# Kernel tuning notes

Hardware: AMD Instinct MI355X
Metric: run time of the kernel (lower is better)

Reference implementation:

```python
import jax, jax.numpy as jnp
import numpy as np

N = 50000   # total residue nodes across the batch of peptides
E = 800000  # total directed intra-peptide edges (avg degree 16)
D = 512


def _w(k, shape):
    fan_in = shape[0]
    return (jax.random.normal(k, shape, jnp.float32) / np.sqrt(fan_in)).astype(jnp.float32)


def setup_inputs() -> dict:
    key = jax.random.key(0)
    ks = jax.random.split(key, 12)
    return {
        "peptide_feature": jax.random.normal(ks[0], (N, D), jnp.float32),
        "edge_index": jax.random.randint(ks[1], (2, E), 0, N),
        # aanet_proj: 512 -> 1024 -> 1024 -> 512 -> 80 (ReLU between, none after last)
        "W1": _w(ks[2], (512, 1024)), "b1": jnp.zeros((1024,), jnp.float32),
        "W2": _w(ks[3], (1024, 1024)), "b2": jnp.zeros((1024,), jnp.float32),
        "W3": _w(ks[4], (1024, 512)), "b3": jnp.zeros((512,), jnp.float32),
        "W4": _w(ks[5], (512, 80)), "b4": jnp.zeros((80,), jnp.float32),
        # in_net: 80 -> 512
        "Win": _w(ks[6], (80, 512)), "bin_": jnp.zeros((512,), jnp.float32),
        # GIN conv MLP: 512 -> 512 -> 512 (eps = 0)
        "Wg1": _w(ks[7], (512, 512)), "bg1": jnp.zeros((512,), jnp.float32),
        "Wg2": _w(ks[8], (512, 512)), "bg2": jnp.zeros((512,), jnp.float32),
        # out_net: 512 -> 80
        "Wout": _w(ks[9], (512, 80)), "bout": jnp.zeros((80,), jnp.float32),
    }


def reference(peptide_feature, edge_index, W1, b1, W2, b2, W3, b3, W4, b4,
              Win, bin_, Wg1, bg1, Wg2, bg2, Wout, bout):
    relu = jax.nn.relu
    # aanet_proj
    h = relu(peptide_feature @ W1 + b1)
    h = relu(h @ W2 + b2)
    h = relu(h @ W3 + b3)
    peptide_feat = h @ W4 + b4                      # [N, 80]
    # in_net
    x = peptide_feat @ Win + bin_                   # [N, 512]
    # GIN message passing (sum aggregation, eps=0): per-sample loop in the
    # original is equivalent to one global pass since edges are sample-local.
    src, dst = edge_index[0], edge_index[1]
    agg = jax.ops.segment_sum(x[src], dst, num_segments=N)   # [N, 512]
    g = x + agg
    g = relu(g @ Wg1 + bg1) @ Wg2 + bg2             # GIN MLP
    # out_net
    peptide_mask = g @ Wout + bout                  # [N, 80]
    return peptide_mask, peptide_feat
```

## Files before the change

### kernel.cpp

```cpp
#include <hip/hip_runtime.h>
#include <stdint.h>


using bf16x8 = __attribute__((ext_vector_type(8))) short;
using f32x4  = __attribute__((ext_vector_type(4))) float;

__device__ inline unsigned short f2bf(float f) {
    union { float f; unsigned u; } v; v.f = f;
    unsigned u = v.u;
    u += 0x7FFFu + ((u >> 16) & 1u);
    return (unsigned short)(u >> 16);
}
__device__ inline float bf2f(unsigned u16) {
    return __uint_as_float(u16 << 16);
}

struct PreDescs {
    const float* W[8]; unsigned short* Wt[8];
    int K[8], M[8], Kp[8], ntx[8], start[8];
    int tEnd, cEnd, eEnd;
    const float* feat; unsigned short* featb; int nFeat;
    const int* ei; int E; int* cnt;
};

__global__ __launch_bounds__(256) void rg_preprocess(PreDescs d) {
    int b = blockIdx.x;
    int tid = threadIdx.x;
    if (b < d.tEnd) {
        __shared__ float t[32][33];
        int di = 0;
#pragma unroll
        for (int i = 1; i < 8; ++i) if (b >= d.start[i]) di = i;
        int local = b - d.start[di];
        int bx = local % d.ntx[di];
        int by = local / d.ntx[di];
        const float* W = d.W[di];
        unsigned short* Wt = d.Wt[di];
        int K = d.K[di], M = d.M[di], Kp = d.Kp[di];
        int mb = bx * 32, kb = by * 32;
        int tx = tid & 31, tg = tid >> 5;
#pragma unroll
        for (int p = 0; p < 4; ++p) {
            int r = tg + p * 8;
            int k = kb + r, m = mb + tx;
            t[r][tx] = (k < K && m < M) ? W[(size_t)k * M + m] : 0.f;
        }
        __syncthreads();
#pragma unroll
        for (int p = 0; p < 4; ++p) {
            int r = tg + p * 8;
            int mo = mb + r, ko = kb + tx;
            Wt[(size_t)mo * Kp + ko] = f2bf(t[tx][r]);
        }
    } else if (b < d.cEnd) {
        int i = ((b - d.tEnd) * 256 + tid) * 4;
        if (i + 3 < d.nFeat) {
            float4 v = *(const float4*)(d.feat + i);
            ushort4 o; o.x = f2bf(v.x); o.y = f2bf(v.y); o.z = f2bf(v.z); o.w = f2bf(v.w);
            *(ushort4*)(d.featb + i) = o;
        }
    } else {
        int e = (b - d.cEnd) * 256 + tid;
        if (e < d.E) atomicAdd(&d.cnt[d.ei[d.E + e]], 1);
    }
}

template <bool RELU, bool OUT_BF, bool OUT_F32, bool DEGB, int MT>
__global__ __launch_bounds__(256) void rg_gemm(
    const unsigned short* __restrict__ A, const unsigned short* __restrict__ Bt,
    const float* __restrict__ bias, const int* __restrict__ deg, int Mvalid,
    unsigned short* __restrict__ outB, float* __restrict__ outF,
    int Nrows, int Kp, int Mp, int gN)
{
    __shared__ __align__(16) unsigned short As[128 * 64];
    __shared__ __align__(16) unsigned short Bs[128 * 64];

    int bid = blockIdx.x;
    int xcd = bid & 7;
    int slot = bid >> 3;
    int c = slot % MT;
    int rsub = slot / MT;
    int rt = rsub * 8 + xcd;
    if (rt >= gN) return;
    const int rowBase = rt * 128;
    const int nBase   = c * 128;

    const int tid  = threadIdx.x;
    const int lane = tid & 63;
    const int w    = tid >> 6;
    const int wm   = w & 1, wn = w >> 1;

    f32x4 acc[4][4];
#pragma unroll
    for (int i = 0; i < 4; ++i)
#pragma unroll
        for (int j = 0; j < 4; ++j) acc[i][j] = (f32x4){0.f, 0.f, 0.f, 0.f};

    const int nkt = Kp >> 6;
    for (int kt = 0; kt < nkt; ++kt) {
        __syncthreads();
        const int k0 = kt * 64;
#pragma unroll
        for (int i = 0; i < 4; ++i) {
            int q   = i * 256 + tid;
            int r   = q >> 3;
            int cbg = (q & 7) ^ (r & 7);
            const unsigned short* gp = A + (size_t)(rowBase + r) * Kp + k0 + cbg * 8;
            __builtin_amdgcn_global_load_lds(
                (const __attribute__((address_space(1))) void*)gp,
                (__attribute__((address_space(3))) void*)(&As[q * 8]), 16, 0, 0);
        }
#pragma unroll
        for (int i = 0; i < 4; ++i) {
            int q   = i * 256 + tid;
            int r   = q >> 3;
            int cbg = (q & 7) ^ (r & 7);
            const unsigned short* gp = Bt + (size_t)(nBase + r) * Kp + k0 + cbg * 8;
            __builtin_amdgcn_global_load_lds(
                (const __attribute__((address_space(1))) void*)gp,
                (__attribute__((address_space(3))) void*)(&Bs[q * 8]), 16, 0, 0);
        }
        __syncthreads();
#pragma unroll
        for (int kk = 0; kk < 2; ++kk) {
            bf16x8 a[4], b[4];
            const int cb = kk * 4 + (lane >> 4);
#pragma unroll
            for (int i = 0; i < 4; ++i) {
                int r = wm * 64 + i * 16 + (lane & 15);
                a[i] = *(const bf16x8*)&As[(r * 8 + (cb ^ (r & 7))) * 8];
            }
#pragma unroll
            for (int j = 0; j < 4; ++j) {
                int r = wn * 64 + j * 16 + (lane & 15);
                b[j] = *(const bf16x8*)&Bs[(r * 8 + (cb ^ (r & 7))) * 8];
            }
#pragma unroll
            for (int i = 0; i < 4; ++i)
#pragma unroll
                for (int j = 0; j < 4; ++j)
                    acc[i][j] = __builtin_amdgcn_mfma_f32_16x16x32_bf16(b[j], a[i], acc[i][j], 0, 0, 0);
        }
    }

    const int quad = lane >> 4;
#pragma unroll
    for (int i = 0; i < 4; ++i) {
        int row = rowBase + wm * 64 + i * 16 + (lane & 15);
        if (row >= Nrows) continue;
        float sc = 1.f;
        if (DEGB) sc = 1.f + (float)deg[row];
#pragma unroll
        for (int j = 0; j < 4; ++j) {
            int colb = nBase + wn * 64 + j * 16 + quad * 4;
            float4 bv = (colb < Mvalid) ? *(const float4*)(bias + colb)
                                        : (float4){0.f, 0.f, 0.f, 0.f};
            float v0 = acc[i][j][0] + sc * bv.x;
            float v1 = acc[i][j][1] + sc * bv.y;
            float v2 = acc[i][j][2] + sc * bv.z;
            float v3 = acc[i][j][3] + sc * bv.w;
            if (RELU) {
                v0 = v0 > 0.f ? v0 : 0.f; v1 = v1 > 0.f ? v1 : 0.f;
                v2 = v2 > 0.f ? v2 : 0.f; v3 = v3 > 0.f ? v3 : 0.f;
            }
            if (OUT_BF) {
                ushort4 o; o.x = f2bf(v0); o.y = f2bf(v1); o.z = f2bf(v2); o.w = f2bf(v3);
                *(ushort4*)(outB + (size_t)row * Mp + colb) = o;
            }
            if (OUT_F32) {
                if (colb < Mvalid)
                    *(float4*)(outF + (size_t)row * Mvalid + colb) = (float4){v0, v1, v2, v3};
            }
        }
    }
}

__device__ __forceinline__ void rg_gridbar(int* bar, int nb, int phase) {
    __syncthreads();
    if (threadIdx.x == 0) {
        __threadfence();
        atomicAdd(bar, 1);
        int target = phase * nb;
        while (__hip_atomic_load(bar, __ATOMIC_RELAXED, __HIP_MEMORY_SCOPE_AGENT) < target) {}
        __threadfence();
    }
    __syncthreads();
}

__global__ __launch_bounds__(1024) void rg_scan_all(
    const int* __restrict__ cnt, int* __restrict__ rowptr, int* __restrict__ cursor,
    int* __restrict__ bsums, int* bar, int Nn, int E, int nb)
{
    __shared__ int sd[1024];
    const int tid = threadIdx.x;
    const int bid = blockIdx.x;
    const int i   = bid * 1024 + tid;

    int v = (i < Nn) ? cnt[i] : 0;
    sd[tid] = v;
    __syncthreads();
    for (int off = 1; off < 1024; off <<= 1) {
        int t = (tid >= off) ? sd[tid - off] : 0;
        __syncthreads();
        sd[tid] += t;
        __syncthreads();
    }
    if (tid == 1023) bsums[bid] = sd[1023];
    rg_gridbar(bar, nb, 1);

    if (bid == 0 && tid < 64) {
        int bv = (tid < nb) ? bsums[tid] : 0;
        int incl = bv;
#pragma unroll
        for (int off = 1; off < 64; off <<= 1) {
            int t = __shfl_up(incl, off, 64);
            if (tid >= off) incl += t;
        }
        if (tid < nb) bsums[tid] = incl - bv;
    }
    rg_gridbar(bar, nb, 2);

    if (i < Nn) {
        int ex = sd[tid] - v + bsums[bid];
        rowptr[i] = ex; cursor[i] = ex;
    }
    if (i == 0) rowptr[Nn] = E;
}

__global__ void rg_scatter_edges(const int* __restrict__ ei, int E,
                                 int* __restrict__ cursor, int* __restrict__ cols) {
    int e = blockIdx.x * 256 + threadIdx.x;
    if (e < E) {
        int d = ei[E + e];
        int p = atomicAdd(&cursor[d], 1);
        cols[p] = ei[e];
    }
}

__global__ __launch_bounds__(256) void rg_agg80(
    const unsigned short* __restrict__ pf, const int* __restrict__ rowptr,
    const int* __restrict__ cols, unsigned short* __restrict__ s, int Nn)
{
    int node = blockIdx.x * 4 + (threadIdx.x >> 6);
    if (node >= Nn) return;
    int lane = threadIdx.x & 63;
    const unsigned* xp = (const unsigned*)pf;
    size_t off = (size_t)node * 64 + lane;
    unsigned u = xp[off];
    float a0 = bf2f(u & 0xffffu), a1 = bf2f(u >> 16);
    int beg = rowptr[node], end = rowptr[node + 1];
    int e = beg;
    for (; e + 8 <= end; e += 8) {
        unsigned v[8];
#pragma unroll
        for (int t = 0; t < 8; ++t) v[t] = xp[(size_t)cols[e + t] * 64 + lane];
#pragma unroll
        for (int t = 0; t < 8; ++t) { a0 += bf2f(v[t] & 0xffffu); a1 += bf2f(v[t] >> 16); }
    }
    for (; e < end; ++e) {
        unsigned v = xp[(size_t)cols[e] * 64 + lane];
        a0 += bf2f(v & 0xffffu); a1 += bf2f(v >> 16);
    }
    unsigned o = (unsigned)f2bf(a0) | ((unsigned)f2bf(a1) << 16);
    ((unsigned*)s)[off] = o;
}

extern "C" void kernel_launch(void* const* d_in, const int* in_sizes, int n_in,
                              void* d_out, int out_size, void* d_ws, size_t ws_size,
                              hipStream_t stream)
{
    const float* feat = (const float*)d_in[0];
    const int*   ei   = (const int*)d_in[1];
    const float* W1 = (const float*)d_in[2];  const float* b1 = (const float*)d_in[3];
    const float* W2 = (const float*)d_in[4];  const float* b2 = (const float*)d_in[5];
    const float* W3 = (const float*)d_in[6];  const float* b3 = (const float*)d_in[7];
    const float* W4 = (const float*)d_in[8];  const float* b4 = (const float*)d_in[9];
    const float* Wi = (const float*)d_in[10]; const float* bi = (const float*)d_in[11];
    const float* Wg1 = (const float*)d_in[12]; const float* bg1 = (const float*)d_in[13];
    const float* Wg2 = (const float*)d_in[14]; const float* bg2 = (const float*)d_in[15];
    const float* Wo = (const float*)d_in[16]; const float* bo = (const float*)d_in[17];

    const int N = in_sizes[0] / 512;
    const int E = in_sizes[1] / 2;
    const int gN = (N + 127) / 128;
    const int Npad = gN * 128;

    char* ws = (char*)d_ws;
    size_t o = 0;
    auto alloc = [&](size_t bytes) { char* p = ws + o; o += (bytes + 255) & ~(size_t)255; return p; };
    unsigned short* bufA = (unsigned short*)alloc((size_t)Npad * 1024 * 2);
    unsigned short* bufB = (unsigned short*)alloc((size_t)Npad * 1024 * 2);
    unsigned short* bufC = (unsigned short*)alloc((size_t)Npad * 512 * 2);
    unsigned short* W1t = (unsigned short*)alloc((size_t)1024 * 512 * 2);
    unsigned short* W2t = (unsigned short*)alloc((size_t)1024 * 1024 * 2);
    unsigned short* W3t = (unsigned short*)alloc((size_t)512 * 1024 * 2);
    unsigned short* W4t = (unsigned short*)alloc((size_t)128 * 512 * 2);
    unsigned short* Wit = (unsigned short*)alloc((size_t)512 * 128 * 2);
    unsigned short* Wg1t = (unsigned short*)alloc((size_t)512 * 512 * 2);
    unsigned short* Wg2t = (unsigned short*)alloc((size_t)512 * 512 * 2);
    unsigned short* Wot = (unsigned short*)alloc((size_t)128 * 512 * 2);
    int* cnt    = (int*)alloc((size_t)(N + 64) * 4);
    int* bar    = cnt + N;
    int* rowptr = (int*)alloc((size_t)(N + 1) * 4);
    int* cursor = (int*)alloc((size_t)N * 4);
    int* cols   = (int*)alloc((size_t)E * 4);
    int* bsums  = (int*)alloc(256);

    float* out_mask = (float*)d_out;
    float* out_feat = (float*)d_out + (size_t)N * 80;

    hipMemsetAsync(cnt, 0, (size_t)(N + 64) * 4, stream);
    {
        PreDescs d;
        const float* Ws[8]  = {W1, W2, W3, W4, Wi, Wg1, Wg2, Wo};
        unsigned short* Ts[8] = {W1t, W2t, W3t, W4t, Wit, Wg1t, Wg2t, Wot};
        int Ks[8]  = {512, 1024, 1024, 512, 80, 512, 512, 512};
        int Ms[8]  = {1024, 1024, 512, 80, 512, 512, 512, 80};
        int Kps[8] = {512, 1024, 1024, 512, 128, 512, 512, 512};
        int Mps[8] = {1024, 1024, 512, 128, 512, 512, 512, 128};
        int st = 0;
        for (int i = 0; i < 8; ++i) {
            d.W[i] = Ws[i]; d.Wt[i] = Ts[i];
            d.K[i] = Ks[i]; d.M[i] = Ms[i]; d.Kp[i] = Kps[i];
            d.ntx[i] = Mps[i] / 32;
            d.start[i] = st;
            st += (Mps[i] / 32) * (Kps[i] / 32);
        }
        d.tEnd = st;
        d.cEnd = st + (N * 512) / 1024;
        d.eEnd = d.cEnd + (E + 255) / 256;
        d.feat = feat; d.featb = bufC; d.nFeat = N * 512;
        d.ei = ei; d.E = E; d.cnt = cnt;
        rg_preprocess<<<d.eEnd, 256, 0, stream>>>(d);
    }

    const int nb = (N + 1023) / 1024;
    rg_scan_all<<<nb, 1024, 0, stream>>>(cnt, rowptr, cursor, bsums, bar, N, E, nb);
    rg_scatter_edges<<<(E + 255) / 256, 256, 0, stream>>>(ei, E, cursor, cols);

    const int rg8 = ((gN + 7) / 8) * 8;
    auto grid = [&](int MT) { return dim3(rg8 * MT); };

    rg_gemm<true, true, false, false, 8><<<grid(8), 256, 0, stream>>>(bufC, W1t, b1, nullptr, 1024, bufA, nullptr, N, 512, 1024, gN);

    {
        const int halfTiles = (gN + 1) / 2;
        const int halfRows  = halfTiles * 128;
        const int gNb       = gN - halfTiles;
        const int rg8a = ((halfTiles + 7) / 8) * 8;
        const int rg8b = ((gNb + 7) / 8) * 8;
        rg_gemm<true, true, false, false, 8><<<dim3(rg8a * 8), 256, 0, stream>>>(
            bufA, W2t, b2, nullptr, 1024, bufB, nullptr, halfRows, 1024, 1024, halfTiles);
        rg_gemm<true, true, false, false, 8><<<dim3(rg8b * 8), 256, 0, stream>>>(
            bufA + (size_t)halfRows * 1024, W2t, b2, nullptr, 1024,
            bufB + (size_t)halfRows * 1024, nullptr, N - halfRows, 1024, 1024, gNb);
    }

    rg_gemm<true, true, false, false, 4><<<grid(4), 256, 0, stream>>>(bufB, W3t, b3, nullptr, 512, bufC, nullptr, N, 1024, 512, gN);
    rg_gemm<false, true, true, false, 1><<<grid(1), 256, 0, stream>>>(bufC, W4t, b4, nullptr, 80, bufA, out_feat, N, 512, 128, gN);

    rg_agg80<<<(N + 3) / 4, 256, 0, stream>>>(bufA, rowptr, cols, bufC, N);

    rg_gemm<false, true, false, true, 4><<<grid(4), 256, 0, stream>>>(bufC, Wit, bi, cnt, 512, bufA, nullptr, N, 128, 512, gN);
    rg_gemm<true, true, false, false, 4><<<grid(4), 256, 0, stream>>>(bufA, Wg1t, bg1, nullptr, 512, bufB, nullptr, N, 512, 512, gN);
    rg_gemm<false, true, false, false, 4><<<grid(4), 256, 0, stream>>>(bufB, Wg2t, bg2, nullptr, 512, bufC, nullptr, N, 512, 512, gN);
    rg_gemm<false, false, true, false, 1><<<grid(1), 256, 0, stream>>>(bufC, Wot, bo, nullptr, 80, nullptr, out_mask, N, 512, 128, gN);
}
```

Baseline: 848.4 us.

## Fuse edge scatter into first GEMM launch and merge split W2 GEMM

Moves the CSR edge-scatter work into extra blocks appended to the first MLP GEMM launch, so the scatter's atomics run alongside the GEMM tiles instead of as a separate kernel. It also replaces the two half-sized W2 GEMM launches with a single full-size launch. Both changes cut kernel launches and let independent work share the GPU. The cost is that scatter blocks compete with GEMM blocks for resources and may sit behind them in the dispatch order, and the single W2 launch changes the tail behaviour.

Measured after the change: 782.9 us. -7.7%, faster.

```diff
diff --git a/kernel.cpp b/kernel.cpp
--- a/kernel.cpp
+++ b/kernel.cpp
@@ -66,7 +66,8 @@
 }
 
 template <bool RELU, bool OUT_BF, bool OUT_F32, bool DEGB, int MT>
-__global__ __launch_bounds__(256) void rg_gemm(
+__device__ __forceinline__ void gemm_body(
+    int bid,
     const unsigned short* __restrict__ A, const unsigned short* __restrict__ Bt,
     const float* __restrict__ bias, const int* __restrict__ deg, int Mvalid,
     unsigned short* __restrict__ outB, float* __restrict__ outF,
@@ -75,7 +76,6 @@
     __shared__ __align__(16) unsigned short As[128 * 64];
     __shared__ __align__(16) unsigned short Bs[128 * 64];
 
-    int bid = blockIdx.x;
     int xcd = bid & 7;
     int slot = bid >> 3;
     int c = slot % MT;
@@ -175,6 +175,38 @@
     }
 }
 
+template <bool RELU, bool OUT_BF, bool OUT_F32, bool DEGB, int MT>
+__global__ __launch_bounds__(256) void rg_gemm(
+    const unsigned short* __restrict__ A, const unsigned short* __restrict__ Bt,
+    const float* __restrict__ bias, const int* __restrict__ deg, int Mvalid,
+    unsigned short* __restrict__ outB, float* __restrict__ outF,
+    int Nrows, int Kp, int Mp, int gN)
+{
+    gemm_body<RELU, OUT_BF, OUT_F32, DEGB, MT>(blockIdx.x, A, Bt, bias, deg,
+                                               Mvalid, outB, outF, Nrows, Kp, Mp, gN);
+}
+
+__global__ __launch_bounds__(256) void rg_gemm_l1_scatter(
+    const unsigned short* __restrict__ A, const unsigned short* __restrict__ Bt,
+    const float* __restrict__ bias, int Mvalid,
+    unsigned short* __restrict__ outB, int Nrows, int Kp, int Mp, int gN,
+    int gemmBlocks, const int* __restrict__ ei, int E,
+    int* __restrict__ cursor, int* __restrict__ cols)
+{
+    int bid = blockIdx.x;
+    if (bid < gemmBlocks) {
+        gemm_body<true, true, false, false, 8>(bid, A, Bt, bias, nullptr,
+                                               Mvalid, outB, nullptr, Nrows, Kp, Mp, gN);
+    } else {
+        int e = (bid - gemmBlocks) * 256 + threadIdx.x;
+        if (e < E) {
+            int d = ei[E + e];
+            int p = atomicAdd(&cursor[d], 1);
+            cols[p] = ei[e];
+        }
+    }
+}
+
 __device__ __forceinline__ void rg_gridbar(int* bar, int nb, int phase) {
     __syncthreads();
     if (threadIdx.x == 0) {
@@ -225,16 +257,6 @@
         rowptr[i] = ex; cursor[i] = ex;
     }
     if (i == 0) rowptr[Nn] = E;
-}
-
-__global__ void rg_scatter_edges(const int* __restrict__ ei, int E,
-                                 int* __restrict__ cursor, int* __restrict__ cols) {
-    int e = blockIdx.x * 256 + threadIdx.x;
-    if (e < E) {
-        int d = ei[E + e];
-        int p = atomicAdd(&cursor[d], 1);
-        cols[p] = ei[e];
-    }
 }
 
 __global__ __launch_bounds__(256) void rg_agg80(
@@ -336,26 +358,19 @@
 
     const int nb = (N + 1023) / 1024;
     rg_scan_all<<<nb, 1024, 0, stream>>>(cnt, rowptr, cursor, bsums, bar, N, E, nb);
-    rg_scatter_edges<<<(E + 255) / 256, 256, 0, stream>>>(ei, E, cursor, cols);
 
     const int rg8 = ((gN + 7) / 8) * 8;
     auto grid = [&](int MT) { return dim3(rg8 * MT); };
 
-    rg_gemm<true, true, false, false, 8><<<grid(8), 256, 0, stream>>>(bufC, W1t, b1, nullptr, 1024, bufA, nullptr, N, 512, 1024, gN);
-
     {
-        const int halfTiles = (gN + 1) / 2;
-        const int halfRows  = halfTiles * 128;
-        const int gNb       = gN - halfTiles;
-        const int rg8a = ((halfTiles + 7) / 8) * 8;
-        const int rg8b = ((gNb + 7) / 8) * 8;
-        rg_gemm<true, true, false, false, 8><<<dim3(rg8a * 8), 256, 0, stream>>>(
-            bufA, W2t, b2, nullptr, 1024, bufB, nullptr, halfRows, 1024, 1024, halfTiles);
-        rg_gemm<true, true, false, false, 8><<<dim3(rg8b * 8), 256, 0, stream>>>(
-            bufA + (size_t)halfRows * 1024, W2t, b2, nullptr, 1024,
-            bufB + (size_t)halfRows * 1024, nullptr, N - halfRows, 1024, 1024, gNb);
-    }
-
+        const int gemmBlocks = rg8 * 8;
+        const int scatBlocks = (E + 255) / 256;
+        rg_gemm_l1_scatter<<<dim3(gemmBlocks + scatBlocks), 256, 0, stream>>>(
+            bufC, W1t, b1, 1024, bufA, N, 512, 1024, gN,
+            gemmBlocks, ei, E, cursor, cols);
+    }
+
+    rg_gemm<true, true, false, false, 8><<<grid(8), 256, 0, stream>>>(bufA, W2t, b2, nullptr, 1024, bufB, nullptr, N, 1024, 1024, gN);
     rg_gemm<true, true, false, false, 4><<<grid(4), 256, 0, stream>>>(bufB, W3t, b3, nullptr, 512, bufC, nullptr, N, 1024, 512, gN);
     rg_gemm<false, true, true, false, 1><<<grid(1), 256, 0, stream>>>(bufC, W4t, b4, nullptr, 80, bufA, out_feat, N, 512, 128, gN);
 
```
